# Performance work log

Measured on AMD Instinct MI355X. Metric: run time of the kernel, lower is better.

The kernel has to match this reference:

```python
import jax, jax.numpy as jnp
import numpy as np

LN_EPS = 1e-5  # torch LayerNorm default


def setup_inputs() -> dict:
    key = jax.random.key(0)
    ks = jax.random.split(key, 6)
    N, E, D = 50000, 800000, 128
    x = jax.random.normal(ks[0], (N, D), dtype=jnp.float32)
    edge_index = jax.random.randint(ks[1], (2, E), 0, N, dtype=jnp.int64)
    # Linear params (torch default-ish init scale)
    W = jax.random.normal(ks[2], (D, D), dtype=jnp.float32) / np.sqrt(D)
    b = jax.random.normal(ks[3], (D,), dtype=jnp.float32) * 0.01
    # LayerNorm params
    gamma = jnp.ones((D,), dtype=jnp.float32)
    beta = jnp.zeros((D,), dtype=jnp.float32)
    return {"x": x, "edge_index": edge_index, "W": W, "b": b,
            "gamma": gamma, "beta": beta}


def reference(x, edge_index, W, b, gamma, beta):
    N = x.shape[0]
    # add_self_loops
    loops = jnp.arange(N, dtype=edge_index.dtype)
    row = jnp.concatenate([edge_index[0], loops])  # sources (x_j)
    col = jnp.concatenate([edge_index[1], loops])  # targets (aggregate here)

    h = x @ W.T + b  # [N, D]

    # symmetric normalization: deg computed on row, includes self loops (deg>=1)
    deg = jax.ops.segment_sum(jnp.ones(row.shape, dtype=h.dtype), row,
                              num_segments=N)
    dis = deg ** -0.5
    norm = dis[row] * dis[col]  # [E+N]

    # gather-scale-scatter message passing (aggr='add')
    msg = norm[:, None] * h[row]              # [E+N, D]
    agg = jax.ops.segment_sum(msg, col, num_segments=N)  # [N, D]

    out = jax.nn.relu(agg)
    # dropout: identity (eval mode)
    mu = jnp.mean(out, axis=-1, keepdims=True)
    var = jnp.var(out, axis=-1, keepdims=True)
    out = (out - mu) * jax.lax.rsqrt(var + LN_EPS) * gamma + beta
    return out + x  # residual (in_channels == out_channels, no proj)
```

## Files before the change

kernel.cpp:

```cpp
#include <hip/hip_runtime.h>


#define D 128
#define CHSH 15
#define CHUNK (1 << CHSH)
#define NWORD 12500

typedef short bf16x8 __attribute__((ext_vector_type(8)));
typedef float f32x4 __attribute__((ext_vector_type(4)));

__device__ __forceinline__ unsigned short f2bf(float f) {
    unsigned u = __float_as_uint(f);
    return (unsigned short)((u + 0x7fffu + ((u >> 16) & 1u)) >> 16);
}
__device__ __forceinline__ float bf2f_lo(unsigned v) { return __uint_as_float(v << 16); }
__device__ __forceinline__ float bf2f_hi(unsigned v) { return __uint_as_float(v & 0xffff0000u); }

__global__ void __launch_bounds__(1024)
k_gemm_hist(const float* __restrict__ x, const float* __restrict__ W,
            const float* __restrict__ bias, unsigned short* __restrict__ hb,
            int nrows,
            const int* __restrict__ ei, int E, int n,
            unsigned char* __restrict__ degc, unsigned char* __restrict__ cntc,
            unsigned char* __restrict__ aux, unsigned* __restrict__ partial, int K) {
    __shared__ unsigned sm[NWORD];
    int bid = blockIdx.x;
    if (bid < 2 * K) {
        if (bid == 0 && threadIdx.x < 256) partial[threadIdx.x] = 0u;
        unsigned* hist = sm;
        bool is_cnt = bid < K;
        int c = is_cnt ? bid : bid - K;
        const int* vs = is_cnt ? (ei + E) : ei;
        for (int i = threadIdx.x; i < NWORD; i += 1024) hist[i] = 0u;
        __syncthreads();
        int e0 = c << CHSH;
        int e1 = e0 + CHUNK; if (e1 > E) e1 = E;
        if (is_cnt) {
            for (int e = e0 + threadIdx.x; e < e1; e += 1024) {
                int v = vs[e];
                unsigned sh = (v & 3) * 8;
                unsigned old = atomicAdd(&hist[v >> 2], 1u << sh);
                aux[e] = (unsigned char)(old >> sh);
            }
        } else {
            for (int e = e0 + threadIdx.x; e < e1; e += 1024) {
                int v = vs[e];
                atomicAdd(&hist[v >> 2], 1u << ((v & 3) * 8));
            }
        }
        __syncthreads();
        unsigned* dst = (unsigned*)((is_cnt ? cntc : degc) + (size_t)c * n);
        for (int i = threadIdx.x; i < NWORD; i += 1024) dst[i] = hist[i];
    } else {
        unsigned short* wf = (unsigned short*)sm;
        for (int s = threadIdx.x; s < D * D; s += 1024) {
            int j  = s & 7;
            int ln = (s >> 3) & 63;
            int g  = s >> 9;
            int kt = g & 3, nt = g >> 2;
            int rw = nt * 16 + (ln & 15);
            int cl = kt * 32 + (ln >> 4) * 8 + j;
            wf[s] = f2bf(W[rw * D + cl]);
        }
        __syncthreads();

        int wid = threadIdx.x >> 6, lane = threadIdx.x & 63;
        int m0 = (bid - 2 * K) * 256 + wid * 16;
        if (m0 >= nrows) return;
        int lo16 = lane & 15, quad = lane >> 4;
        const float* arow = x + (size_t)(m0 + lo16) * D + quad * 8;
        bf16x8 a[4];
        #pragma unroll
        for (int kt = 0; kt < 4; kt++) {
            float4 p = *(const float4*)(arow + kt * 32);
            float4 q = *(const float4*)(arow + kt * 32 + 4);
            bf16x8 av;
            av[0] = (short)f2bf(p.x); av[1] = (short)f2bf(p.y);
            av[2] = (short)f2bf(p.z); av[3] = (short)f2bf(p.w);
            av[4] = (short)f2bf(q.x); av[5] = (short)f2bf(q.y);
            av[6] = (short)f2bf(q.z); av[7] = (short)f2bf(q.w);
            a[kt] = av;
        }
        const bf16x8* wfv = (const bf16x8*)sm;
        #pragma unroll
        for (int nt = 0; nt < 8; nt++) {
            int n0 = nt * 16;
            float bj = bias[n0 + lo16];
            f32x4 acc = {bj, bj, bj, bj};
            #pragma unroll
            for (int kt = 0; kt < 4; kt++) {
                bf16x8 b = wfv[(nt * 4 + kt) * 64 + lane];
                acc = __builtin_amdgcn_mfma_f32_16x16x32_bf16(a[kt], b, acc, 0, 0, 0);
            }
            #pragma unroll
            for (int r = 0; r < 4; r++) {
                int gr = m0 + quad * 4 + r;
                hb[(size_t)gr * D + n0 + lo16] = f2bf(acc[r]);
            }
        }
    }
}

__global__ void k_scan(const unsigned char* __restrict__ degc,
                       const unsigned char* __restrict__ cntc,
                       float* __restrict__ dis, int* __restrict__ rowptr,
                       unsigned char* __restrict__ pre8,
                       unsigned* __restrict__ partial, int n, int E, int K) {
    __shared__ unsigned ps[256];
    __shared__ unsigned bb_sh;
    int t = threadIdx.x, bid = blockIdx.x;
    int i = bid * 256 + t;
    unsigned tot = 0;
    if (i < n) {
        unsigned d = 0;
        for (int c = 0; c < K; c++)
            d += __builtin_nontemporal_load(degc + (size_t)c * n + i);
        dis[i] = rsqrtf((float)d + 1.0f);
        unsigned run = 0;
        for (int c = 0; c < K; c++) {
            pre8[(size_t)c * n + i] = (unsigned char)run;
            run += cntc[(size_t)c * n + i];
        }
        tot = run;
    }
    ps[t] = tot;
    __syncthreads();
    #pragma unroll
    for (int d = 1; d < 256; d <<= 1) {
        unsigned u = (t >= d) ? ps[t - d] : 0u;
        __syncthreads();
        ps[t] += u;
        __syncthreads();
    }
    unsigned incl = ps[t];
    unsigned agg  = ps[255];
    if (t < 64) {
        if (t == 0) atomicExch(&partial[bid], agg | 0x80000000u);
        unsigned sum = 0;
        for (int j0 = 0; j0 < bid; j0 += 64) {
            int j = j0 + t;
            if (j < bid) {
                unsigned v;
                do { v = atomicAdd(&partial[j], 0u); } while (!(v & 0x80000000u));
                sum += v & 0x7fffffffu;
            }
        }
        #pragma unroll
        for (int mm = 32; mm >= 1; mm >>= 1) sum += __shfl_xor(sum, mm, 64);
        if (t == 0) bb_sh = sum;
    }
    __syncthreads();
    unsigned bbase = bb_sh;
    if (i < n) rowptr[i] = (int)(bbase + incl - tot);
    if (bid == 0 && t == 0) rowptr[n] = E;
}

__global__ void k_fill(const int* __restrict__ ei, int E, int n,
                       const int* __restrict__ rowptr, const unsigned char* __restrict__ pre8,
                       const unsigned char* __restrict__ aux,
                       unsigned short* __restrict__ srcs) {
    int e = blockIdx.x * 256 + threadIdx.x;
    if (e < E) {
        int r = __builtin_nontemporal_load(ei + e);
        int v = __builtin_nontemporal_load(ei + E + e);
        int c = e >> CHSH;
        int rank = __builtin_nontemporal_load(aux + e);
        int base = rowptr[v] + (int)pre8[(size_t)c * n + v];
        srcs[base + rank] = (unsigned short)r;
    }
}

__global__ void k_agg(const float* __restrict__ x, const unsigned short* __restrict__ hb,
                      const float* __restrict__ dis,
                      const int* __restrict__ rowptr, const unsigned short* __restrict__ srcs,
                      const float* __restrict__ gamma, const float* __restrict__ beta,
                      float* __restrict__ out, int n) {
    int wid = threadIdx.x >> 6, lane = threadIdx.x & 63;
    int row = blockIdx.x * 4 + wid;
    if (row >= n) return;
    int q = lane >> 4, t = lane & 15;
    float dc = dis[row];
    float acc[8];
    #pragma unroll
    for (int i = 0; i < 8; i++) acc[i] = 0.0f;
    if (q == 0) {
        uint4 u = ((const uint4*)(hb + (size_t)row * D))[t];
        float sn = dc * dc;
        acc[0] = sn * bf2f_lo(u.x); acc[1] = sn * bf2f_hi(u.x);
        acc[2] = sn * bf2f_lo(u.y); acc[3] = sn * bf2f_hi(u.y);
        acc[4] = sn * bf2f_lo(u.z); acc[5] = sn * bf2f_hi(u.z);
        acc[6] = sn * bf2f_lo(u.w); acc[7] = sn * bf2f_hi(u.w);
    }
    int s0 = rowptr[row];
    int len = rowptr[row + 1] - s0;
    for (int base = 0; base < len; base += 64) {
        int idx = base + lane;
        int sv = (idx < len) ? (int)__builtin_nontemporal_load(srcs + s0 + idx) : 0;
        float dv = (idx < len) ? dis[sv] : 0.0f;
        int m = len - base; if (m > 64) m = 64;
        int kmax = (m + 3) >> 2;
        int gcount = (kmax + 3) >> 2;
        for (int gg = 0; gg < gcount; gg++) {
            int jb = q + (gg << 4);
            int r0 = __shfl(sv, jb, 64);
            int r1 = __shfl(sv, jb + 4, 64);
            int r2 = __shfl(sv, jb + 8, 64);
            int r3 = __shfl(sv, jb + 12, 64);
            float w0 = dc * __shfl(dv, jb, 64);
            float w1 = dc * __shfl(dv, jb + 4, 64);
            float w2 = dc * __shfl(dv, jb + 8, 64);
            float w3 = dc * __shfl(dv, jb + 12, 64);
            uint4 u0 = ((const uint4*)(hb + ((size_t)r0 << 7)))[t];
            uint4 u1 = ((const uint4*)(hb + ((size_t)r1 << 7)))[t];
            uint4 u2 = ((const uint4*)(hb + ((size_t)r2 << 7)))[t];
            uint4 u3 = ((const uint4*)(hb + ((size_t)r3 << 7)))[t];
            acc[0] += w0 * bf2f_lo(u0.x); acc[1] += w0 * bf2f_hi(u0.x);
            acc[2] += w0 * bf2f_lo(u0.y); acc[3] += w0 * bf2f_hi(u0.y);
            acc[4] += w0 * bf2f_lo(u0.z); acc[5] += w0 * bf2f_hi(u0.z);
            acc[6] += w0 * bf2f_lo(u0.w); acc[7] += w0 * bf2f_hi(u0.w);
            acc[0] += w1 * bf2f_lo(u1.x); acc[1] += w1 * bf2f_hi(u1.x);
            acc[2] += w1 * bf2f_lo(u1.y); acc[3] += w1 * bf2f_hi(u1.y);
            acc[4] += w1 * bf2f_lo(u1.z); acc[5] += w1 * bf2f_hi(u1.z);
            acc[6] += w1 * bf2f_lo(u1.w); acc[7] += w1 * bf2f_hi(u1.w);
            acc[0] += w2 * bf2f_lo(u2.x); acc[1] += w2 * bf2f_hi(u2.x);
            acc[2] += w2 * bf2f_lo(u2.y); acc[3] += w2 * bf2f_hi(u2.y);
            acc[4] += w2 * bf2f_lo(u2.z); acc[5] += w2 * bf2f_hi(u2.z);
            acc[6] += w2 * bf2f_lo(u2.w); acc[7] += w2 * bf2f_hi(u2.w);
            acc[0] += w3 * bf2f_lo(u3.x); acc[1] += w3 * bf2f_hi(u3.x);
            acc[2] += w3 * bf2f_lo(u3.y); acc[3] += w3 * bf2f_hi(u3.y);
            acc[4] += w3 * bf2f_lo(u3.z); acc[5] += w3 * bf2f_hi(u3.z);
            acc[6] += w3 * bf2f_lo(u3.w); acc[7] += w3 * bf2f_hi(u3.w);
        }
    }
    #pragma unroll
    for (int i = 0; i < 8; i++) {
        acc[i] += __shfl_xor(acc[i], 16, 64);
        acc[i] += __shfl_xor(acc[i], 32, 64);
        acc[i] = acc[i] > 0.0f ? acc[i] : 0.0f;
    }
    float s1r = 0.0f, s2r = 0.0f;
    #pragma unroll
    for (int i = 0; i < 8; i++) { s1r += acc[i]; s2r += acc[i] * acc[i]; }
    #pragma unroll
    for (int mm = 8; mm >= 1; mm >>= 1) {
        s1r += __shfl_xor(s1r, mm, 64);
        s2r += __shfl_xor(s2r, mm, 64);
    }
    float mean = s1r * (1.0f / 128.0f);
    float var  = s2r * (1.0f / 128.0f) - mean * mean;
    float rstd = rsqrtf(var + 1e-5f);
    if (q == 0) {
        const f32x4* gr = (const f32x4*)gamma;
        const f32x4* br = (const f32x4*)beta;
        const f32x4* xr = (const f32x4*)(x + (size_t)row * D);
        f32x4* orow = (f32x4*)(out + (size_t)row * D);
        #pragma unroll
        for (int hf = 0; hf < 2; hf++) {
            f32x4 g = gr[2 * t + hf], b = br[2 * t + hf];
            f32x4 xx = __builtin_nontemporal_load(xr + 2 * t + hf);
            f32x4 o;
            o[0] = (acc[4 * hf + 0] - mean) * rstd * g[0] + b[0] + xx[0];
            o[1] = (acc[4 * hf + 1] - mean) * rstd * g[1] + b[1] + xx[1];
            o[2] = (acc[4 * hf + 2] - mean) * rstd * g[2] + b[2] + xx[2];
            o[3] = (acc[4 * hf + 3] - mean) * rstd * g[3] + b[3] + xx[3];
            __builtin_nontemporal_store(o, orow + 2 * t + hf);
        }
    }
}

extern "C" void kernel_launch(void* const* d_in, const int* in_sizes, int n_in,
                              void* d_out, int out_size, void* d_ws, size_t ws_size,
                              hipStream_t stream) {
    const float* x     = (const float*)d_in[0];
    const int*   ei    = (const int*)d_in[1];
    const float* W     = (const float*)d_in[2];
    const float* bias  = (const float*)d_in[3];
    const float* gamma = (const float*)d_in[4];
    const float* beta  = (const float*)d_in[5];
    int N = in_sizes[0] / D;
    int E = in_sizes[1] / 2;
    int nb  = (N + 255) / 256;
    int nbE = (E + 255) / 256;
    int K   = (E + CHUNK - 1) >> CHSH;
    int gemm_blocks = (N + 255) / 256;

    char* ws = (char*)d_ws;
    size_t off = 0;
    unsigned short* hb  = (unsigned short*)(ws + off); off += (size_t)N * D * 2;
    unsigned char* degc = (unsigned char*)(ws + off);  off += (size_t)K * N;
    unsigned char* cntc = (unsigned char*)(ws + off);  off += (size_t)K * N;
    float*    dis       = (float*)(ws + off);          off += (size_t)N * 4;
    int*      rowptr    = (int*)(ws + off);            off += (size_t)(N + 1) * 4;
    unsigned char* pre8 = (unsigned char*)(ws + off);  off += (size_t)K * N;
    unsigned* partial   = (unsigned*)(ws + off);       off += 256 * 4;
    unsigned char* aux  = (unsigned char*)(ws + off);  off += (size_t)E;
    off = (off + 1) & ~(size_t)1;
    unsigned short* srcs = (unsigned short*)(ws + off); off += (size_t)E * 2;
    float*    out       = (float*)d_out;

    k_gemm_hist<<<2 * K + gemm_blocks, 1024, 0, stream>>>(x, W, bias, hb, N,
                                                          ei, E, N, degc, cntc, aux,
                                                          partial, K);
    k_scan<<<nb, 256, 0, stream>>>(degc, cntc, dis, rowptr, pre8, partial, N, E, K);
    k_fill<<<nbE, 256, 0, stream>>>(ei, E, N, rowptr, pre8, aux, srcs);
    k_agg<<<(N + 3) / 4, 256, 0, stream>>>(x, hb, dis, rowptr, srcs, gamma, beta, out, N);
}
```

Baseline: 174.1 us.

## Fuse degree/rowptr scan into histogram+GEMM kernel via atomic completion counter

The separate scan kernel is folded into the combined histogram/GEMM launch as trailing blocks that spin on a global done counter until all histogram blocks finish. The scan now uses 1024-thread blocks, so only 49 blocks exist and the decoupled lookback collapses to a single per-lane read. A memset replaces the in-kernel zeroing of partial and also clears the counter. The aim is to remove one kernel launch boundary and let the scan overlap with the GEMM blocks. In exchange it relies on the scan blocks being scheduled after the histogram blocks and adds busy-wait spinning plus an extra memset operation.

```diff
diff --git a/kernel.cpp b/kernel.cpp
--- a/kernel.cpp
+++ b/kernel.cpp
@@ -22,38 +22,45 @@
             int nrows,
             const int* __restrict__ ei, int E, int n,
             unsigned char* __restrict__ degc, unsigned char* __restrict__ cntc,
-            unsigned char* __restrict__ aux, unsigned* __restrict__ partial, int K) {
+            unsigned char* __restrict__ aux,
+            float* __restrict__ dis, int* __restrict__ rowptr,
+            unsigned char* __restrict__ pre8,
+            unsigned* __restrict__ partial, unsigned* __restrict__ done,
+            int K, int gemm_blocks) {
     __shared__ unsigned sm[NWORD];
     int bid = blockIdx.x;
+    int t = threadIdx.x;
     if (bid < 2 * K) {
-        if (bid == 0 && threadIdx.x < 256) partial[threadIdx.x] = 0u;
         unsigned* hist = sm;
         bool is_cnt = bid < K;
         int c = is_cnt ? bid : bid - K;
         const int* vs = is_cnt ? (ei + E) : ei;
-        for (int i = threadIdx.x; i < NWORD; i += 1024) hist[i] = 0u;
+        for (int i = t; i < NWORD; i += 1024) hist[i] = 0u;
         __syncthreads();
         int e0 = c << CHSH;
         int e1 = e0 + CHUNK; if (e1 > E) e1 = E;
         if (is_cnt) {
-            for (int e = e0 + threadIdx.x; e < e1; e += 1024) {
+            for (int e = e0 + t; e < e1; e += 1024) {
                 int v = vs[e];
                 unsigned sh = (v & 3) * 8;
                 unsigned old = atomicAdd(&hist[v >> 2], 1u << sh);
                 aux[e] = (unsigned char)(old >> sh);
             }
         } else {
-            for (int e = e0 + threadIdx.x; e < e1; e += 1024) {
+            for (int e = e0 + t; e < e1; e += 1024) {
                 int v = vs[e];
                 atomicAdd(&hist[v >> 2], 1u << ((v & 3) * 8));
             }
         }
         __syncthreads();
         unsigned* dst = (unsigned*)((is_cnt ? cntc : degc) + (size_t)c * n);
-        for (int i = threadIdx.x; i < NWORD; i += 1024) dst[i] = hist[i];
-    } else {
+        for (int i = t; i < NWORD; i += 1024) dst[i] = hist[i];
+        __threadfence();
+        __syncthreads();
+        if (t == 0) atomicAdd(done, 1u);
+    } else if (bid < 2 * K + gemm_blocks) {
         unsigned short* wf = (unsigned short*)sm;
-        for (int s = threadIdx.x; s < D * D; s += 1024) {
+        for (int s = t; s < D * D; s += 1024) {
             int j  = s & 7;
             int ln = (s >> 3) & 63;
             int g  = s >> 9;
@@ -64,7 +71,7 @@
         }
         __syncthreads();
 
-        int wid = threadIdx.x >> 6, lane = threadIdx.x & 63;
+        int wid = t >> 6, lane = t & 63;
         int m0 = (bid - 2 * K) * 256 + wid * 16;
         if (m0 >= nrows) return;
         int lo16 = lane & 15, quad = lane >> 4;
@@ -98,61 +105,55 @@
                 hb[(size_t)gr * D + n0 + lo16] = f2bf(acc[r]);
             }
         }
-    }
-}
-
-__global__ void k_scan(const unsigned char* __restrict__ degc,
-                       const unsigned char* __restrict__ cntc,
-                       float* __restrict__ dis, int* __restrict__ rowptr,
-                       unsigned char* __restrict__ pre8,
-                       unsigned* __restrict__ partial, int n, int E, int K) {
-    __shared__ unsigned ps[256];
-    __shared__ unsigned bb_sh;
-    int t = threadIdx.x, bid = blockIdx.x;
-    int i = bid * 256 + t;
-    unsigned tot = 0;
-    if (i < n) {
-        unsigned d = 0;
-        for (int c = 0; c < K; c++)
-            d += __builtin_nontemporal_load(degc + (size_t)c * n + i);
-        dis[i] = rsqrtf((float)d + 1.0f);
-        unsigned run = 0;
-        for (int c = 0; c < K; c++) {
-            pre8[(size_t)c * n + i] = (unsigned char)run;
-            run += cntc[(size_t)c * n + i];
-        }
-        tot = run;
-    }
-    ps[t] = tot;
-    __syncthreads();
-    #pragma unroll
-    for (int d = 1; d < 256; d <<= 1) {
-        unsigned u = (t >= d) ? ps[t - d] : 0u;
-        __syncthreads();
-        ps[t] += u;
-        __syncthreads();
-    }
-    unsigned incl = ps[t];
-    unsigned agg  = ps[255];
-    if (t < 64) {
-        if (t == 0) atomicExch(&partial[bid], agg | 0x80000000u);
-        unsigned sum = 0;
-        for (int j0 = 0; j0 < bid; j0 += 64) {
-            int j = j0 + t;
-            if (j < bid) {
+    } else {
+        int sid = bid - 2 * K - gemm_blocks;
+        __shared__ unsigned bb_sh;
+        if (t == 0) {
+            while (atomicAdd(done, 0u) < 2u * (unsigned)K) {}
+        }
+        __syncthreads();
+        __threadfence();
+        int i = sid * 1024 + t;
+        unsigned tot = 0;
+        if (i < n) {
+            unsigned d = 0;
+            for (int c = 0; c < K; c++)
+                d += __builtin_nontemporal_load(degc + (size_t)c * n + i);
+            dis[i] = rsqrtf((float)d + 1.0f);
+            unsigned run = 0;
+            for (int c = 0; c < K; c++) {
+                pre8[(size_t)c * n + i] = (unsigned char)run;
+                run += cntc[(size_t)c * n + i];
+            }
+            tot = run;
+        }
+        sm[t] = tot;
+        __syncthreads();
+        for (int d = 1; d < 1024; d <<= 1) {
+            unsigned u = (t >= d) ? sm[t - d] : 0u;
+            __syncthreads();
+            sm[t] += u;
+            __syncthreads();
+        }
+        unsigned incl = sm[t];
+        unsigned agg  = sm[1023];
+        if (t < 64) {
+            if (t == 0) atomicExch(&partial[sid], agg | 0x80000000u);
+            unsigned sum = 0;
+            if (t < sid) {
                 unsigned v;
-                do { v = atomicAdd(&partial[j], 0u); } while (!(v & 0x80000000u));
-                sum += v & 0x7fffffffu;
-            }
-        }
-        #pragma unroll
-        for (int mm = 32; mm >= 1; mm >>= 1) sum += __shfl_xor(sum, mm, 64);
-        if (t == 0) bb_sh = sum;
-    }
-    __syncthreads();
-    unsigned bbase = bb_sh;
-    if (i < n) rowptr[i] = (int)(bbase + incl - tot);
-    if (bid == 0 && t == 0) rowptr[n] = E;
+                do { v = atomicAdd(&partial[t], 0u); } while (!(v & 0x80000000u));
+                sum = v & 0x7fffffffu;
+            }
+            #pragma unroll
+            for (int mm = 32; mm >= 1; mm >>= 1) sum += __shfl_xor(sum, mm, 64);
+            if (t == 0) bb_sh = sum;
+        }
+        __syncthreads();
+        unsigned bbase = bb_sh;
+        if (i < n) rowptr[i] = (int)(bbase + incl - tot);
+        if (sid == 0 && t == 0) rowptr[n] = E;
+    }
 }
 
 __global__ void k_fill(const int* __restrict__ ei, int E, int n,
@@ -279,10 +280,10 @@
     const float* beta  = (const float*)d_in[5];
     int N = in_sizes[0] / D;
     int E = in_sizes[1] / 2;
-    int nb  = (N + 255) / 256;
     int nbE = (E + 255) / 256;
     int K   = (E + CHUNK - 1) >> CHSH;
     int gemm_blocks = (N + 255) / 256;
+    int nscan = (N + 1023) / 1024;
 
     char* ws = (char*)d_ws;
     size_t off = 0;
@@ -293,15 +294,17 @@
     int*      rowptr    = (int*)(ws + off);            off += (size_t)(N + 1) * 4;
     unsigned char* pre8 = (unsigned char*)(ws + off);  off += (size_t)K * N;
     unsigned* partial   = (unsigned*)(ws + off);       off += 256 * 4;
+    unsigned* done      = (unsigned*)(ws + off);       off += 64;
     unsigned char* aux  = (unsigned char*)(ws + off);  off += (size_t)E;
     off = (off + 1) & ~(size_t)1;
     unsigned short* srcs = (unsigned short*)(ws + off); off += (size_t)E * 2;
     float*    out       = (float*)d_out;
 
-    k_gemm_hist<<<2 * K + gemm_blocks, 1024, 0, stream>>>(x, W, bias, hb, N,
-                                                          ei, E, N, degc, cntc, aux,
-                                                          partial, K);
-    k_scan<<<nb, 256, 0, stream>>>(degc, cntc, dis, rowptr, pre8, partial, N, E, K);
+    hipMemsetAsync(partial, 0, 256 * 4 + 64, stream);
+
+    k_gemm_hist<<<2 * K + gemm_blocks + nscan, 1024, 0, stream>>>(
+        x, W, bias, hb, N, ei, E, N, degc, cntc, aux,
+        dis, rowptr, pre8, partial, done, K, gemm_blocks);
     k_fill<<<nbE, 256, 0, stream>>>(ei, E, N, rowptr, pre8, aux, srcs);
     k_agg<<<(N + 3) / 4, 256, 0, stream>>>(x, hb, dis, rowptr, srcs, gamma, beta, out, N);
 }
```

Measured after the change: 212.4 us. +22.0%, slower.
